# Kernel tuning notes

Measured on AMD Instinct MI355X. Metric: run time of the kernel, lower is better.

The kernel has to match this reference:

```python
import jax, jax.numpy as jnp
import numpy as np

N_NODES = 50000
N_EDGES = 600000
DIM = 128
NGC = 3
NMC = 2
B = 64
M_PER = 100
M_TOT = B * M_PER
EM = 50000
DICT = 201  # motif_dict_size + 1


def setup_inputs() -> dict:
    key = jax.random.key(0)
    ks = jax.random.split(key, 20)
    w = lambda k, s: jax.random.normal(k, s, jnp.float32) * 0.05
    x = jax.random.normal(ks[0], (N_NODES, DIM), jnp.float32)
    edge_attr = jax.random.normal(ks[1], (N_EDGES, DIM), jnp.float32)
    edge_index = jax.random.randint(ks[2], (2, N_EDGES), 0, N_NODES)
    batch = jnp.sort(jax.random.randint(ks[3], (N_NODES,), 0, B))
    node2motif = jax.random.randint(ks[4], (N_NODES,), 0, M_PER)
    num_motifs = jnp.full((B,), M_PER, dtype=jnp.int32)  # fill 'ones' * 100
    # ring over all motifs guarantees unique(motif_edge_index) == 0..M_TOT-1,
    # so the original node_idx relabel is the identity map
    ring = jnp.stack([jnp.arange(M_TOT), (jnp.arange(M_TOT) + 1) % M_TOT])
    rnd = jax.random.randint(ks[5], (2, EM - M_TOT), 0, M_TOT)
    motif_edge_index = jnp.concatenate([ring, rnd], axis=1).astype(jnp.int32)
    motifid = jax.random.randint(ks[6], (M_TOT,), 0, DICT)
    emb = w(ks[7], (DICT, DIM)).at[0].set(0.0)  # padding_idx=0 row zeroed
    return dict(
        x=x, edge_attr=edge_attr, edge_index=edge_index, batch=batch,
        node2motif=node2motif, num_motifs=num_motifs,
        motif_edge_index=motif_edge_index, motifid=motifid,
        gc_W1=w(ks[8], (NGC, DIM, DIM)), gc_b1=jnp.zeros((NGC, DIM)),
        gc_W2=w(ks[9], (NGC, DIM, DIM)), gc_b2=jnp.zeros((NGC, DIM)),
        mc_W1=w(ks[10], (NMC, DIM, DIM)), mc_b1=jnp.zeros((NMC, DIM)),
        mc_W2=w(ks[11], (NMC, DIM, DIM)), mc_b2=jnp.zeros((NMC, DIM)),
        lin_W=w(ks[12], (DIM * NGC, DIM)), lin_b=jnp.zeros((DIM,)),
        emb=emb,
    )


def reference(x, edge_attr, edge_index, batch, node2motif, num_motifs,
              motif_edge_index, motifid,
              gc_W1, gc_b1, gc_W2, gc_b2,
              mc_W1, mc_b1, mc_W2, mc_b2,
              lin_W, lin_b, emb):
    N = x.shape[0]
    src, dst = edge_index[0], edge_index[1]
    # --- GINE conv stack (eps=0, no norm, dropout=0) ---
    xg_list = []
    for i in range(NGC):
        msg = jax.nn.relu(x[src] + edge_attr)                 # [E, dim]
        agg = jax.ops.segment_sum(msg, dst, num_segments=N)   # [N, dim]
        h = x + agg
        h = jax.nn.relu(h @ gc_W1[i] + gc_b1[i]) @ gc_W2[i] + gc_b2[i]
        x = jax.nn.relu(h)
        xg_list.append(x)
    xcat = jnp.concatenate(xg_list, axis=1)                   # [N, dim*NGC]
    xg = jax.ops.segment_sum(xcat, batch, num_segments=B)     # [B, dim*NGC]
    # --- motif grouping ---
    partial = jnp.concatenate([jnp.zeros((1,), num_motifs.dtype),
                               jnp.cumsum(num_motifs)[:-1]])
    n2m = node2motif + partial[batch]                         # [N] -> motif ids
    # injective=False: motif_lin first, then pool
    xm_nodes = jax.nn.relu(xcat @ lin_W + lin_b)              # [N, dim]
    xm_h = jax.ops.segment_sum(xm_nodes, n2m, num_segments=M_TOT)
    motif_batch = jnp.repeat(jnp.arange(B), num_motifs, total_repeat_length=M_TOT)
    # motif_edge_index covers exactly 0..M_TOT-1, so relabel is identity
    msrc, mdst = motif_edge_index[0], motif_edge_index[1]
    xm_h = xm_h + emb[motifid]
    # --- GIN conv stack on motif graph ---
    xm_list = []
    h = xm_h
    for i in range(NMC):
        agg = jax.ops.segment_sum(h[msrc], mdst, num_segments=M_TOT)
        t = h + agg
        t = jax.nn.relu(t @ mc_W1[i] + mc_b1[i]) @ mc_W2[i] + mc_b2[i]
        h = jax.nn.relu(t)
        xm_list.append(h)
    xm = jnp.concatenate(xm_list, axis=1)                     # [M_TOT, dim*NMC]
    xm = jax.ops.segment_sum(xm, motif_batch, num_segments=B) # [B, dim*NMC]
    return xm, xg
```

## Files before the change

### kernel.cpp

```cpp
#include <hip/hip_runtime.h>

typedef __attribute__((ext_vector_type(8))) short bf16x8;
typedef __attribute__((ext_vector_type(4))) float f32x4;

__device__ __forceinline__ unsigned f2bf_rne(float f) {
  unsigned u = __float_as_uint(f);
  return (u + 0x7FFFu + ((u >> 16) & 1u)) >> 16;
}
__device__ __forceinline__ float bf2f(unsigned h) { return __uint_as_float(h << 16); }
__device__ __forceinline__ void split_bf(float x, unsigned& hi, unsigned& lo) {
  hi = f2bf_rne(x);
  lo = f2bf_rne(x - bf2f(hi));
}

__global__ void prep_kernel(const int* __restrict__ num_motifs,
                            const int* __restrict__ batch,
                            int N, int B,
                            int* __restrict__ partial,
                            int* __restrict__ bnd) {
  int t = threadIdx.x;
  if (t == 0) {
    int s = 0;
    for (int b = 0; b < B; ++b) { partial[b] = s; s += num_motifs[b]; }
  }
  if (t <= B) {
    int lo = 0, hi = N;
    while (lo < hi) { int mid = (lo + hi) >> 1; if (batch[mid] < t) lo = mid + 1; else hi = mid; }
    bnd[t] = lo;
  }
}

__global__ __launch_bounds__(256) void hist_kernel(const int* __restrict__ dst, int E,
                                                   int* __restrict__ counts) {
  int e = blockIdx.x * 256 + threadIdx.x;
  if (e < E) atomicAdd(&counts[dst[e]], 1);
}

__global__ __launch_bounds__(1024) void scan_kernel(const int* __restrict__ counts, int n,
                                                    int* __restrict__ base,
                                                    int* __restrict__ cursor) {
  __shared__ int part[1024];
  const int tid = threadIdx.x;
  const int chunk = (n + 1023) / 1024;
  const int lo = tid * chunk;
  const int hi = min(lo + chunk, n);
  int s = 0;
  for (int i = lo; i < hi; ++i) s += counts[i];
  part[tid] = s;
  __syncthreads();
  for (int off = 1; off < 1024; off <<= 1) {
    int v = (tid >= off) ? part[tid - off] : 0;
    __syncthreads();
    part[tid] += v;
    __syncthreads();
  }
  int run = (tid > 0) ? part[tid - 1] : 0;
  for (int i = lo; i < hi; ++i) {
    base[i] = run; cursor[i] = run;
    run += counts[i];
  }
  if (tid == 1023) base[n] = part[1023];
}

__global__ __launch_bounds__(256) void scatter_kernel(const int* __restrict__ src,
                                                      const int* __restrict__ dst, int E,
                                                      int* __restrict__ cursor,
                                                      int* __restrict__ eid_s,
                                                      int* __restrict__ src_s) {
  int e = blockIdx.x * 256 + threadIdx.x;
  if (e >= E) return;
  int d = dst[e];
  int pos = atomicAdd(&cursor[d], 1);
  eid_s[pos] = e;
  src_s[pos] = src[e];
}

__global__ __launch_bounds__(256) void nm_hist_kernel(const int* __restrict__ n2m,
                                                      const int* __restrict__ batch,
                                                      const int* __restrict__ partial, int N,
                                                      int* __restrict__ counts) {
  int n = blockIdx.x * 256 + threadIdx.x;
  if (n < N) atomicAdd(&counts[n2m[n] + partial[batch[n]]], 1);
}

__global__ __launch_bounds__(256) void nm_scatter_kernel(const int* __restrict__ n2m,
                                                         const int* __restrict__ batch,
                                                         const int* __restrict__ partial, int N,
                                                         int* __restrict__ cursor,
                                                         int* __restrict__ node_s) {
  int n = blockIdx.x * 256 + threadIdx.x;
  if (n >= N) return;
  int m = n2m[n] + partial[batch[n]];
  node_s[atomicAdd(&cursor[m], 1)] = n;
}

__global__ __launch_bounds__(128) void gine_agg_kernel(
    const float* __restrict__ x, const float* __restrict__ ea,
    const int* __restrict__ base, const int* __restrict__ eid_s,
    const int* __restrict__ src_s, float* __restrict__ h, int N) {
  const int n = blockIdx.x * 2 + (threadIdx.x >> 6);
  if (n >= N) return;
  const int d2 = (threadIdx.x & 63) * 2;
  const int e0 = base[n], e1 = base[n + 1];
  float sx = 0.f, sy = 0.f;
  int j = e0;
  for (; j + 1 < e1; j += 2) {
    int eA = eid_s[j],     sA = src_s[j];
    int eB = eid_s[j + 1], sB = src_s[j + 1];
    float2 xa = *(const float2*)&x[sA * 128 + d2];
    float2 ja = *(const float2*)&ea[(long long)eA * 128 + d2];
    float2 xb = *(const float2*)&x[sB * 128 + d2];
    float2 jb = *(const float2*)&ea[(long long)eB * 128 + d2];
    sx += fmaxf(xa.x + ja.x, 0.f) + fmaxf(xb.x + jb.x, 0.f);
    sy += fmaxf(xa.y + ja.y, 0.f) + fmaxf(xb.y + jb.y, 0.f);
  }
  if (j < e1) {
    float2 xa = *(const float2*)&x[src_s[j] * 128 + d2];
    float2 ja = *(const float2*)&ea[(long long)eid_s[j] * 128 + d2];
    sx += fmaxf(xa.x + ja.x, 0.f);
    sy += fmaxf(xa.y + ja.y, 0.f);
  }
  float2 xv = *(const float2*)&x[n * 128 + d2];
  *(float2*)&h[n * 128 + d2] = make_float2(xv.x + sx, xv.y + sy);
}

__global__ __launch_bounds__(128) void gin_agg_kernel(
    const float* __restrict__ hi, const int* __restrict__ base,
    const int* __restrict__ src_s, float* __restrict__ ho, int M) {
  const int m = blockIdx.x * 2 + (threadIdx.x >> 6);
  if (m >= M) return;
  const int d2 = (threadIdx.x & 63) * 2;
  const int e0 = base[m], e1 = base[m + 1];
  float sx = 0.f, sy = 0.f;
  int j = e0;
  for (; j + 1 < e1; j += 2) {
    float2 a = *(const float2*)&hi[src_s[j] * 128 + d2];
    float2 b = *(const float2*)&hi[src_s[j + 1] * 128 + d2];
    sx += a.x + b.x; sy += a.y + b.y;
  }
  if (j < e1) {
    float2 a = *(const float2*)&hi[src_s[j] * 128 + d2];
    sx += a.x; sy += a.y;
  }
  float2 hv = *(const float2*)&hi[m * 128 + d2];
  *(float2*)&ho[m * 128 + d2] = make_float2(hv.x + sx, hv.y + sy);
}

__global__ __launch_bounds__(128) void motif_gather_kernel(
    const float* __restrict__ xm_nodes, const int* __restrict__ mb,
    const int* __restrict__ node_s, const int* __restrict__ motifid,
    const float* __restrict__ emb, float* __restrict__ xm_h, int M) {
  const int m = blockIdx.x * 2 + (threadIdx.x >> 6);
  if (m >= M) return;
  const int d2 = (threadIdx.x & 63) * 2;
  float2 e = *(const float2*)&emb[motifid[m] * 128 + d2];
  float sx = e.x, sy = e.y;
  const int j0 = mb[m], j1 = mb[m + 1];
  int j = j0;
  for (; j + 1 < j1; j += 2) {
    float2 a = *(const float2*)&xm_nodes[(long long)node_s[j] * 128 + d2];
    float2 b = *(const float2*)&xm_nodes[(long long)node_s[j + 1] * 128 + d2];
    sx += a.x + b.x; sy += a.y + b.y;
  }
  if (j < j1) {
    float2 a = *(const float2*)&xm_nodes[(long long)node_s[j] * 128 + d2];
    sx += a.x; sy += a.y;
  }
  *(float2*)&xm_h[m * 128 + d2] = make_float2(sx, sy);
}

struct WSrc { const float* p[13]; };

__global__ __launch_bounds__(256) void convw_kernel(WSrc wsrc, ushort* __restrict__ Wf) {
  const int mat = blockIdx.x >> 2;
  const int kc  = blockIdx.x & 3;
  const float* W = wsrc.p[mat];
  const int t = threadIdx.x;
  #pragma unroll
  for (int i = 0; i < 16; ++i) {
    int o = t * 16 + i;
    int nt = o >> 9, lane = (o >> 3) & 63, j = o & 7;
    int k = kc * 32 + (lane >> 4) * 8 + j;
    int n = nt * 16 + (lane & 15);
    unsigned hi, lo;
    split_bf(W[k * 128 + n], hi, lo);
    Wf[mat * 32768 + kc * 4096 + o]         = (ushort)hi;
    Wf[mat * 32768 + 16384 + kc * 4096 + o] = (ushort)lo;
  }
}

__device__ __forceinline__ void stage_a_bf(ushort* AsH, ushort* AsL,
                                           const float* __restrict__ src,
                                           int row0, int nrows, int tid) {
  #pragma unroll
  for (int it = 0; it < 16; ++it) {
    int idx = (it * 256 + tid) * 4;
    int r = idx >> 7, k = idx & 127;
    float4 v = make_float4(0.f, 0.f, 0.f, 0.f);
    if (row0 + r < nrows) v = *(const float4*)&src[(long long)(row0 + r) * 128 + k];
    unsigned h0, l0, h1, l1, h2, l2, h3, l3;
    split_bf(v.x, h0, l0); split_bf(v.y, h1, l1);
    split_bf(v.z, h2, l2); split_bf(v.w, h3, l3);
    uint2 ph = make_uint2(h0 | (h1 << 16), h2 | (h3 << 16));
    uint2 pl = make_uint2(l0 | (l1 << 16), l2 | (l3 << 16));
    int boff = r * 256 + ((k * 2) ^ ((r & 7) << 4));
    *(uint2*)((char*)AsH + boff) = ph;
    *(uint2*)((char*)AsL + boff) = pl;
  }
}

__device__ __forceinline__ bf16x8 ld_afrag(const ushort* As, int row, int k0) {
  int boff = row * 256 + ((k0 * 2) ^ ((row & 7) << 4));
  return *(const bf16x8*)((const char*)As + boff);
}

__device__ __forceinline__ bf16x8 ld_wfrag(const ushort* Wf, int kc, int nt, int lane) {
  return ((const bf16x8*)Wf)[(kc * 8 + nt) * 64 + lane];
}

__device__ __forceinline__ void mfma_gemm(const ushort* AsH, const ushort* AsL,
                                          const ushort* WfH, const ushort* WfL,
                                          int wr, int wc, int lane, f32x4 (&acc)[4][4]) {
  #pragma unroll
  for (int kc = 0; kc < 4; ++kc) {
    const int k0 = kc * 32 + (lane >> 4) * 8;
    bf16x8 ah[4], al[4], wh[4], wl[4];
    #pragma unroll
    for (int rt = 0; rt < 4; ++rt) {
      int row = wr * 64 + rt * 16 + (lane & 15);
      ah[rt] = ld_afrag(AsH, row, k0);
      al[rt] = ld_afrag(AsL, row, k0);
    }
    #pragma unroll
    for (int ct = 0; ct < 4; ++ct) {
      int nt = wc * 4 + ct;
      wh[ct] = ld_wfrag(WfH, kc, nt, lane);
      wl[ct] = ld_wfrag(WfL, kc, nt, lane);
    }
    #pragma unroll
    for (int rt = 0; rt < 4; ++rt)
      #pragma unroll
      for (int ct = 0; ct < 4; ++ct) {
        acc[rt][ct] = __builtin_amdgcn_mfma_f32_16x16x32_bf16(ah[rt], wh[ct], acc[rt][ct], 0, 0, 0);
        acc[rt][ct] = __builtin_amdgcn_mfma_f32_16x16x32_bf16(ah[rt], wl[ct], acc[rt][ct], 0, 0, 0);
        acc[rt][ct] = __builtin_amdgcn_mfma_f32_16x16x32_bf16(al[rt], wh[ct], acc[rt][ct], 0, 0, 0);
      }
  }
}

__device__ __forceinline__ void bias_acc(f32x4 (&acc)[4][4], const float* __restrict__ b,
                                         int wc, int lane) {
  #pragma unroll
  for (int ct = 0; ct < 4; ++ct) {
    float bv = b[wc * 64 + ct * 16 + (lane & 15)];
    #pragma unroll
    for (int rt = 0; rt < 4; ++rt) acc[rt][ct] = (f32x4){bv, bv, bv, bv};
  }
}

__global__ __launch_bounds__(256, 2) void mlp_mfma_kernel(
    const float* __restrict__ h,
    const ushort* __restrict__ W1f, const float* __restrict__ b1,
    const ushort* __restrict__ W2f, const float* __restrict__ b2,
    float* __restrict__ out, int nrows) {
  __shared__ ushort AsH[128 * 128];
  __shared__ ushort AsL[128 * 128];
  const int tid = threadIdx.x;
  const int lane = tid & 63;
  const int w = tid >> 6;
  const int wr = w >> 1, wc = w & 1;
  const int row0 = blockIdx.x * 128;

  stage_a_bf(AsH, AsL, h, row0, nrows, tid);
  __syncthreads();

  f32x4 acc[4][4];
  bias_acc(acc, b1, wc, lane);
  mfma_gemm(AsH, AsL, W1f, W1f + 16384, wr, wc, lane, acc);
  __syncthreads();

  #pragma unroll
  for (int rt = 0; rt < 4; ++rt)
    #pragma unroll
    for (int ct = 0; ct < 4; ++ct) {
      int col = wc * 64 + ct * 16 + (lane & 15);
      #pragma unroll
      for (int r = 0; r < 4; ++r) {
        int row = wr * 64 + rt * 16 + (lane >> 4) * 4 + r;
        unsigned hi, lo;
        split_bf(fmaxf(acc[rt][ct][r], 0.f), hi, lo);
        int boff = row * 256 + ((col * 2) ^ ((row & 7) << 4));
        *(ushort*)((char*)AsH + boff) = (ushort)hi;
        *(ushort*)((char*)AsL + boff) = (ushort)lo;
      }
    }
  __syncthreads();

  f32x4 acc2[4][4];
  bias_acc(acc2, b2, wc, lane);
  mfma_gemm(AsH, AsL, W2f, W2f + 16384, wr, wc, lane, acc2);

  #pragma unroll
  for (int rt = 0; rt < 4; ++rt)
    #pragma unroll
    for (int ct = 0; ct < 4; ++ct) {
      int col = wc * 64 + ct * 16 + (lane & 15);
      #pragma unroll
      for (int r = 0; r < 4; ++r) {
        int row = row0 + wr * 64 + rt * 16 + (lane >> 4) * 4 + r;
        if (row < nrows) out[(long long)row * 128 + col] = fmaxf(acc2[rt][ct][r], 0.f);
      }
    }
}

__global__ __launch_bounds__(256, 2) void lin_mfma_kernel(
    const float* __restrict__ x1, const float* __restrict__ x2, const float* __restrict__ x3,
    const ushort* __restrict__ Wlf, const float* __restrict__ lb,
    float* __restrict__ xm_nodes, int nrows) {
  __shared__ ushort AsH[128 * 128];
  __shared__ ushort AsL[128 * 128];
  const int tid = threadIdx.x;
  const int lane = tid & 63;
  const int w = tid >> 6;
  const int wr = w >> 1, wc = w & 1;
  const int row0 = blockIdx.x * 128;

  f32x4 acc[4][4];
  bias_acc(acc, lb, wc, lane);

  for (int c3 = 0; c3 < 3; ++c3) {
    const float* xs = (c3 == 0) ? x1 : (c3 == 1 ? x2 : x3);
    if (c3) __syncthreads();
    stage_a_bf(AsH, AsL, xs, row0, nrows, tid);
    __syncthreads();
    const ushort* Wc = Wlf + c3 * 32768;
    mfma_gemm(AsH, AsL, Wc, Wc + 16384, wr, wc, lane, acc);
  }

  #pragma unroll
  for (int rt = 0; rt < 4; ++rt)
    #pragma unroll
    for (int ct = 0; ct < 4; ++ct) {
      int col = wc * 64 + ct * 16 + (lane & 15);
      #pragma unroll
      for (int r = 0; r < 4; ++r) {
        int row = row0 + wr * 64 + rt * 16 + (lane >> 4) * 4 + r;
        if (row < nrows) xm_nodes[(long long)row * 128 + col] = fmaxf(acc[rt][ct][r], 0.f);
      }
    }
}

__global__ __launch_bounds__(192) void xg_pool_kernel(
    const float* __restrict__ x1, const float* __restrict__ x2, const float* __restrict__ x3,
    const int* __restrict__ batch, int N, int chunk, float* __restrict__ outg) {
  const int c0 = blockIdx.x * chunk;
  if (c0 >= N) return;
  const int c1 = min(c0 + chunk, N);
  const int l = threadIdx.x >> 6;
  const int d2 = (threadIdx.x & 63) * 2;
  const float* xs = (l == 0) ? x1 : (l == 1 ? x2 : x3);
  int b = batch[c0];
  float sx = 0.f, sy = 0.f;
  for (int n = c0; n < c1; ++n) {
    int bn = batch[n];
    if (bn != b) {
      if (sx != 0.f) atomicAdd(&outg[b * 384 + l * 128 + d2], sx);
      if (sy != 0.f) atomicAdd(&outg[b * 384 + l * 128 + d2 + 1], sy);
      sx = 0.f; sy = 0.f; b = bn;
    }
    float2 v = *(const float2*)&xs[n * 128 + d2];
    sx += v.x; sy += v.y;
  }
  atomicAdd(&outg[b * 384 + l * 128 + d2], sx);
  atomicAdd(&outg[b * 384 + l * 128 + d2 + 1], sy);
}

__global__ __launch_bounds__(128) void xm_pool_kernel(
    const float* __restrict__ m1, const float* __restrict__ m2,
    const int* __restrict__ partial, int B, int M, int chunk,
    float* __restrict__ outm) {
  const int c0 = blockIdx.x * chunk;
  if (c0 >= M) return;
  const int c1 = min(c0 + chunk, M);
  const int l = threadIdx.x >> 6;
  const int d2 = (threadIdx.x & 63) * 2;
  const float* ms = (l == 0) ? m1 : m2;
  int b = 0;
  while (b + 1 < B && partial[b + 1] <= c0) ++b;
  int bend = (b + 1 < B) ? partial[b + 1] : M;
  float sx = 0.f, sy = 0.f;
  for (int m = c0; m < c1; ++m) {
    if (m >= bend) {
      if (sx != 0.f) atomicAdd(&outm[b * 256 + l * 128 + d2], sx);
      if (sy != 0.f) atomicAdd(&outm[b * 256 + l * 128 + d2 + 1], sy);
      sx = 0.f; sy = 0.f;
      do { ++b; } while (b + 1 < B && partial[b + 1] <= m);
      bend = (b + 1 < B) ? partial[b + 1] : M;
    }
    float2 v = *(const float2*)&ms[m * 128 + d2];
    sx += v.x; sy += v.y;
  }
  atomicAdd(&outm[b * 256 + l * 128 + d2], sx);
  atomicAdd(&outm[b * 256 + l * 128 + d2 + 1], sy);
}

extern "C" void kernel_launch(void* const* d_in, const int* in_sizes, int n_in,
                              void* d_out, int out_size, void* d_ws, size_t ws_size,
                              hipStream_t stream) {
  const float* x       = (const float*)d_in[0];
  const float* ea      = (const float*)d_in[1];
  const int*   eidx    = (const int*)d_in[2];
  const int*   batch   = (const int*)d_in[3];
  const int*   n2m     = (const int*)d_in[4];
  const int*   nmot    = (const int*)d_in[5];
  const int*   meidx   = (const int*)d_in[6];
  const int*   motifid = (const int*)d_in[7];
  const float* gcW1 = (const float*)d_in[8];
  const float* gcb1 = (const float*)d_in[9];
  const float* gcW2 = (const float*)d_in[10];
  const float* gcb2 = (const float*)d_in[11];
  const float* mcW1 = (const float*)d_in[12];
  const float* mcb1 = (const float*)d_in[13];
  const float* mcW2 = (const float*)d_in[14];
  const float* mcb2 = (const float*)d_in[15];
  const float* linW = (const float*)d_in[16];
  const float* linb = (const float*)d_in[17];
  const float* emb  = (const float*)d_in[18];
  float* outp = (float*)d_out;

  const int N  = in_sizes[0] / 128;
  const int E  = in_sizes[1] / 128;
  const int B  = in_sizes[5];
  const int ME = in_sizes[6] / 2;
  const int M  = in_sizes[7];

  const size_t nodeBytes = (size_t)N * 128 * 4;
  const size_t motBytes  = (size_t)M * 128 * 4;
  char* ws = (char*)d_ws;
  float* xl0 = (float*)ws;                 ws += nodeBytes;
  float* xl1 = (float*)ws;                 ws += nodeBytes;
  float* xl2 = (float*)ws;                 ws += nodeBytes;
  char*  R   = ws;                         ws += nodeBytes;
  ushort* Wf = (ushort*)ws;                ws += (size_t)13 * 32768 * 2;
  int* counts  = (int*)ws;                 ws += (size_t)N * 4;
  int* base    = (int*)ws;                 ws += (size_t)(N + 1) * 4;
  int* cursor  = (int*)ws;                 ws += (size_t)N * 4;
  int* eid_s   = (int*)ws;                 ws += (size_t)E * 4;
  int* src_s   = (int*)ws;                 ws += (size_t)E * 4;
  int* mcounts = (int*)ws;                 ws += (size_t)M * 4;
  int* mbase   = (int*)ws;                 ws += (size_t)(M + 1) * 4;
  int* mcursor = (int*)ws;                 ws += (size_t)M * 4;
  int* meid_s  = (int*)ws;                 ws += (size_t)ME * 4;
  int* msrc_s  = (int*)ws;                 ws += (size_t)ME * 4;
  int* nmcnt   = (int*)ws;                 ws += (size_t)M * 4;
  int* nmbase  = (int*)ws;                 ws += (size_t)(M + 1) * 4;
  int* nmcur   = (int*)ws;                 ws += (size_t)M * 4;
  int* node_s  = (int*)ws;                 ws += (size_t)N * 4;
  int* partial = (int*)ws;                 ws += 256;
  int* bnd     = (int*)ws;                 ws += 512;
  if ((size_t)(ws - (char*)d_ws) > ws_size) return;

  float* hbuf     = (float*)R;
  float* xm_nodes = (float*)R;
  float* xmh = (float*)((char*)xl0);
  float* hm  = (float*)((char*)xl0 + motBytes);
  float* ml0 = (float*)((char*)xl0 + 2 * motBytes);
  float* ml1 = (float*)((char*)xl0 + 3 * motBytes);

  hipMemsetAsync(outp, 0, (size_t)out_size * 4, stream);

  prep_kernel<<<1, 128, 0, stream>>>(nmot, batch, N, B, partial, bnd);

  WSrc wsrc;
  wsrc.p[0] = gcW1;            wsrc.p[1] = gcW1 + 16384;  wsrc.p[2] = gcW1 + 32768;
  wsrc.p[3] = gcW2;            wsrc.p[4] = gcW2 + 16384;  wsrc.p[5] = gcW2 + 32768;
  wsrc.p[6] = mcW1;            wsrc.p[7] = mcW1 + 16384;
  wsrc.p[8] = mcW2;            wsrc.p[9] = mcW2 + 16384;
  wsrc.p[10] = linW;           wsrc.p[11] = linW + 16384; wsrc.p[12] = linW + 32768;
  convw_kernel<<<52, 256, 0, stream>>>(wsrc, Wf);

  const int* src = eidx;
  const int* dst = eidx + E;
  hipMemsetAsync(counts, 0, (size_t)N * 4, stream);
  hist_kernel<<<(E + 255) / 256, 256, 0, stream>>>(dst, E, counts);
  scan_kernel<<<1, 1024, 0, stream>>>(counts, N, base, cursor);
  scatter_kernel<<<(E + 255) / 256, 256, 0, stream>>>(src, dst, E, cursor, eid_s, src_s);

  const int* msrc = meidx;
  const int* mdst = meidx + ME;
  hipMemsetAsync(mcounts, 0, (size_t)M * 4, stream);
  hist_kernel<<<(ME + 255) / 256, 256, 0, stream>>>(mdst, ME, mcounts);
  scan_kernel<<<1, 1024, 0, stream>>>(mcounts, M, mbase, mcursor);
  scatter_kernel<<<(ME + 255) / 256, 256, 0, stream>>>(msrc, mdst, ME, mcursor, meid_s, msrc_s);

  hipMemsetAsync(nmcnt, 0, (size_t)M * 4, stream);
  nm_hist_kernel<<<(N + 255) / 256, 256, 0, stream>>>(n2m, batch, partial, N, nmcnt);
  scan_kernel<<<1, 1024, 0, stream>>>(nmcnt, M, nmbase, nmcur);
  nm_scatter_kernel<<<(N + 255) / 256, 256, 0, stream>>>(n2m, batch, partial, N, nmcur, node_s);

  const float* xs[3] = {x, xl0, xl1};
  float* xo[3] = {xl0, xl1, xl2};
  const int ngrid = (N + 127) / 128;
  for (int i = 0; i < 3; ++i) {
    gine_agg_kernel<<<(N + 1) / 2, 128, 0, stream>>>(xs[i], ea, base, eid_s, src_s, hbuf, N);
    mlp_mfma_kernel<<<ngrid, 256, 0, stream>>>(hbuf,
        Wf + (size_t)(0 + i) * 32768, gcb1 + i * 128,
        Wf + (size_t)(3 + i) * 32768, gcb2 + i * 128, xo[i], N);
  }
  {
    const int nb = 512;
    const int chunk = (N + nb - 1) / nb;
    xg_pool_kernel<<<nb, 192, 0, stream>>>(xl0, xl1, xl2, batch, N, chunk, outp + B * 256);
  }

  lin_mfma_kernel<<<ngrid, 256, 0, stream>>>(xl0, xl1, xl2, Wf + (size_t)10 * 32768, linb,
                                             xm_nodes, N);
  motif_gather_kernel<<<(M + 1) / 2, 128, 0, stream>>>(xm_nodes, nmbase, node_s,
                                                       motifid, emb, xmh, M);

  const float* hs[2] = {xmh, ml0};
  float* mo[2] = {ml0, ml1};
  const int mgrid = (M + 127) / 128;
  for (int i = 0; i < 2; ++i) {
    gin_agg_kernel<<<(M + 1) / 2, 128, 0, stream>>>(hs[i], mbase, msrc_s, hm, M);
    mlp_mfma_kernel<<<mgrid, 256, 0, stream>>>(hm,
        Wf + (size_t)(6 + i) * 32768, mcb1 + i * 128,
        Wf + (size_t)(8 + i) * 32768, mcb2 + i * 128, mo[i], M);
  }
  {
    const int nb = 256;
    const int chunk = (M + nb - 1) / nb;
    xm_pool_kernel<<<nb, 128, 0, stream>>>(ml0, ml1, partial, B, M, chunk, outp);
  }
}
```

Baseline: 1.125 ms.

## Permute edge attributes into CSR order once and reuse across GINE layers

On the first GINE layer, the aggregation kernel writes each gathered edge_attr row into a dst-sorted buffer. Layers two and three then read that buffer sequentially instead of gathering rows by edge id, and unroll the loop by four. Edge id and source index are packed into one int2 array. This turns two random 307MB-scale gathers into streaming reads, at the cost of an extra 307MB write and workspace in the first layer.

```diff
diff --git a/kernel.cpp b/kernel.cpp
--- a/kernel.cpp
+++ b/kernel.cpp
@@ -65,14 +65,12 @@
 __global__ __launch_bounds__(256) void scatter_kernel(const int* __restrict__ src,
                                                       const int* __restrict__ dst, int E,
                                                       int* __restrict__ cursor,
-                                                      int* __restrict__ eid_s,
-                                                      int* __restrict__ src_s) {
+                                                      int2* __restrict__ ed_s) {
   int e = blockIdx.x * 256 + threadIdx.x;
   if (e >= E) return;
   int d = dst[e];
   int pos = atomicAdd(&cursor[d], 1);
-  eid_s[pos] = e;
-  src_s[pos] = src[e];
+  ed_s[pos] = make_int2(e, src[e]);
 }
 
 __global__ __launch_bounds__(256) void nm_hist_kernel(const int* __restrict__ n2m,
@@ -94,10 +92,10 @@
   node_s[atomicAdd(&cursor[m], 1)] = n;
 }
 
-__global__ __launch_bounds__(128) void gine_agg_kernel(
+__global__ __launch_bounds__(128) void gine_first_kernel(
     const float* __restrict__ x, const float* __restrict__ ea,
-    const int* __restrict__ base, const int* __restrict__ eid_s,
-    const int* __restrict__ src_s, float* __restrict__ h, int N) {
+    const int* __restrict__ base, const int2* __restrict__ ed_s,
+    float* __restrict__ ea_s, float* __restrict__ h, int N) {
   const int n = blockIdx.x * 2 + (threadIdx.x >> 6);
   if (n >= N) return;
   const int d2 = (threadIdx.x & 63) * 2;
@@ -105,18 +103,21 @@
   float sx = 0.f, sy = 0.f;
   int j = e0;
   for (; j + 1 < e1; j += 2) {
-    int eA = eid_s[j],     sA = src_s[j];
-    int eB = eid_s[j + 1], sB = src_s[j + 1];
-    float2 xa = *(const float2*)&x[sA * 128 + d2];
-    float2 ja = *(const float2*)&ea[(long long)eA * 128 + d2];
-    float2 xb = *(const float2*)&x[sB * 128 + d2];
-    float2 jb = *(const float2*)&ea[(long long)eB * 128 + d2];
+    int2 eA = ed_s[j], eB = ed_s[j + 1];
+    float2 ja = *(const float2*)&ea[(long long)eA.x * 128 + d2];
+    float2 jb = *(const float2*)&ea[(long long)eB.x * 128 + d2];
+    float2 xa = *(const float2*)&x[eA.y * 128 + d2];
+    float2 xb = *(const float2*)&x[eB.y * 128 + d2];
+    *(float2*)&ea_s[(long long)j * 128 + d2] = ja;
+    *(float2*)&ea_s[(long long)(j + 1) * 128 + d2] = jb;
     sx += fmaxf(xa.x + ja.x, 0.f) + fmaxf(xb.x + jb.x, 0.f);
     sy += fmaxf(xa.y + ja.y, 0.f) + fmaxf(xb.y + jb.y, 0.f);
   }
   if (j < e1) {
-    float2 xa = *(const float2*)&x[src_s[j] * 128 + d2];
-    float2 ja = *(const float2*)&ea[(long long)eid_s[j] * 128 + d2];
+    int2 eA = ed_s[j];
+    float2 ja = *(const float2*)&ea[(long long)eA.x * 128 + d2];
+    float2 xa = *(const float2*)&x[eA.y * 128 + d2];
+    *(float2*)&ea_s[(long long)j * 128 + d2] = ja;
     sx += fmaxf(xa.x + ja.x, 0.f);
     sy += fmaxf(xa.y + ja.y, 0.f);
   }
@@ -124,9 +125,45 @@
   *(float2*)&h[n * 128 + d2] = make_float2(xv.x + sx, xv.y + sy);
 }
 
+__global__ __launch_bounds__(128) void gine_rest_kernel(
+    const float* __restrict__ x, const float* __restrict__ ea_s,
+    const int* __restrict__ base, const int2* __restrict__ ed_s,
+    float* __restrict__ h, int N) {
+  const int n = blockIdx.x * 2 + (threadIdx.x >> 6);
+  if (n >= N) return;
+  const int d2 = (threadIdx.x & 63) * 2;
+  const int e0 = base[n], e1 = base[n + 1];
+  float sx = 0.f, sy = 0.f;
+  int j = e0;
+  for (; j + 3 < e1; j += 4) {
+    int s0 = ed_s[j].y, s1 = ed_s[j + 1].y, s2 = ed_s[j + 2].y, s3 = ed_s[j + 3].y;
+    float2 j0 = *(const float2*)&ea_s[(long long)j * 128 + d2];
+    float2 j1 = *(const float2*)&ea_s[(long long)(j + 1) * 128 + d2];
+    float2 j2 = *(const float2*)&ea_s[(long long)(j + 2) * 128 + d2];
+    float2 j3 = *(const float2*)&ea_s[(long long)(j + 3) * 128 + d2];
+    float2 x0 = *(const float2*)&x[s0 * 128 + d2];
+    float2 x1 = *(const float2*)&x[s1 * 128 + d2];
+    float2 x2 = *(const float2*)&x[s2 * 128 + d2];
+    float2 x3 = *(const float2*)&x[s3 * 128 + d2];
+    sx += fmaxf(x0.x + j0.x, 0.f) + fmaxf(x1.x + j1.x, 0.f)
+        + fmaxf(x2.x + j2.x, 0.f) + fmaxf(x3.x + j3.x, 0.f);
+    sy += fmaxf(x0.y + j0.y, 0.f) + fmaxf(x1.y + j1.y, 0.f)
+        + fmaxf(x2.y + j2.y, 0.f) + fmaxf(x3.y + j3.y, 0.f);
+  }
+  for (; j < e1; ++j) {
+    int s0 = ed_s[j].y;
+    float2 j0 = *(const float2*)&ea_s[(long long)j * 128 + d2];
+    float2 x0 = *(const float2*)&x[s0 * 128 + d2];
+    sx += fmaxf(x0.x + j0.x, 0.f);
+    sy += fmaxf(x0.y + j0.y, 0.f);
+  }
+  float2 xv = *(const float2*)&x[n * 128 + d2];
+  *(float2*)&h[n * 128 + d2] = make_float2(xv.x + sx, xv.y + sy);
+}
+
 __global__ __launch_bounds__(128) void gin_agg_kernel(
     const float* __restrict__ hi, const int* __restrict__ base,
-    const int* __restrict__ src_s, float* __restrict__ ho, int M) {
+    const int2* __restrict__ ed_s, float* __restrict__ ho, int M) {
   const int m = blockIdx.x * 2 + (threadIdx.x >> 6);
   if (m >= M) return;
   const int d2 = (threadIdx.x & 63) * 2;
@@ -134,12 +171,12 @@
   float sx = 0.f, sy = 0.f;
   int j = e0;
   for (; j + 1 < e1; j += 2) {
-    float2 a = *(const float2*)&hi[src_s[j] * 128 + d2];
-    float2 b = *(const float2*)&hi[src_s[j + 1] * 128 + d2];
+    float2 a = *(const float2*)&hi[ed_s[j].y * 128 + d2];
+    float2 b = *(const float2*)&hi[ed_s[j + 1].y * 128 + d2];
     sx += a.x + b.x; sy += a.y + b.y;
   }
   if (j < e1) {
-    float2 a = *(const float2*)&hi[src_s[j] * 128 + d2];
+    float2 a = *(const float2*)&hi[ed_s[j].y * 128 + d2];
     sx += a.x; sy += a.y;
   }
   float2 hv = *(const float2*)&hi[m * 128 + d2];
@@ -441,17 +478,16 @@
   float* xl1 = (float*)ws;                 ws += nodeBytes;
   float* xl2 = (float*)ws;                 ws += nodeBytes;
   char*  R   = ws;                         ws += nodeBytes;
+  float* ea_s = (float*)ws;                ws += (size_t)E * 128 * 4;
   ushort* Wf = (ushort*)ws;                ws += (size_t)13 * 32768 * 2;
   int* counts  = (int*)ws;                 ws += (size_t)N * 4;
   int* base    = (int*)ws;                 ws += (size_t)(N + 1) * 4;
   int* cursor  = (int*)ws;                 ws += (size_t)N * 4;
-  int* eid_s   = (int*)ws;                 ws += (size_t)E * 4;
-  int* src_s   = (int*)ws;                 ws += (size_t)E * 4;
+  int2* ed_s   = (int2*)ws;                ws += (size_t)E * 8;
   int* mcounts = (int*)ws;                 ws += (size_t)M * 4;
   int* mbase   = (int*)ws;                 ws += (size_t)(M + 1) * 4;
   int* mcursor = (int*)ws;                 ws += (size_t)M * 4;
-  int* meid_s  = (int*)ws;                 ws += (size_t)ME * 4;
-  int* msrc_s  = (int*)ws;                 ws += (size_t)ME * 4;
+  int2* med_s  = (int2*)ws;                ws += (size_t)ME * 8;
   int* nmcnt   = (int*)ws;                 ws += (size_t)M * 4;
   int* nmbase  = (int*)ws;                 ws += (size_t)(M + 1) * 4;
   int* nmcur   = (int*)ws;                 ws += (size_t)M * 4;
@@ -484,25 +520,27 @@
   hipMemsetAsync(counts, 0, (size_t)N * 4, stream);
   hist_kernel<<<(E + 255) / 256, 256, 0, stream>>>(dst, E, counts);
   scan_kernel<<<1, 1024, 0, stream>>>(counts, N, base, cursor);
-  scatter_kernel<<<(E + 255) / 256, 256, 0, stream>>>(src, dst, E, cursor, eid_s, src_s);
+  scatter_kernel<<<(E + 255) / 256, 256, 0, stream>>>(src, dst, E, cursor, ed_s);
 
   const int* msrc = meidx;
   const int* mdst = meidx + ME;
   hipMemsetAsync(mcounts, 0, (size_t)M * 4, stream);
   hist_kernel<<<(ME + 255) / 256, 256, 0, stream>>>(mdst, ME, mcounts);
   scan_kernel<<<1, 1024, 0, stream>>>(mcounts, M, mbase, mcursor);
-  scatter_kernel<<<(ME + 255) / 256, 256, 0, stream>>>(msrc, mdst, ME, mcursor, meid_s, msrc_s);
+  scatter_kernel<<<(ME + 255) / 256, 256, 0, stream>>>(msrc, mdst, ME, mcursor, med_s);
 
   hipMemsetAsync(nmcnt, 0, (size_t)M * 4, stream);
   nm_hist_kernel<<<(N + 255) / 256, 256, 0, stream>>>(n2m, batch, partial, N, nmcnt);
   scan_kernel<<<1, 1024, 0, stream>>>(nmcnt, M, nmbase, nmcur);
   nm_scatter_kernel<<<(N + 255) / 256, 256, 0, stream>>>(n2m, batch, partial, N, nmcur, node_s);
 
-  const float* xs[3] = {x, xl0, xl1};
   float* xo[3] = {xl0, xl1, xl2};
   const int ngrid = (N + 127) / 128;
-  for (int i = 0; i < 3; ++i) {
-    gine_agg_kernel<<<(N + 1) / 2, 128, 0, stream>>>(xs[i], ea, base, eid_s, src_s, hbuf, N);
+  gine_first_kernel<<<(N + 1) / 2, 128, 0, stream>>>(x, ea, base, ed_s, ea_s, hbuf, N);
+  mlp_mfma_kernel<<<ngrid, 256, 0, stream>>>(hbuf,
+      Wf + (size_t)0 * 32768, gcb1, Wf + (size_t)3 * 32768, gcb2, xl0, N);
+  for (int i = 1; i < 3; ++i) {
+    gine_rest_kernel<<<(N + 1) / 2, 128, 0, stream>>>(xo[i - 1], ea_s, base, ed_s, hbuf, N);
     mlp_mfma_kernel<<<ngrid, 256, 0, stream>>>(hbuf,
         Wf + (size_t)(0 + i) * 32768, gcb1 + i * 128,
         Wf + (size_t)(3 + i) * 32768, gcb2 + i * 128, xo[i], N);
@@ -522,7 +560,7 @@
   float* mo[2] = {ml0, ml1};
   const int mgrid = (M + 127) / 128;
   for (int i = 0; i < 2; ++i) {
-    gin_agg_kernel<<<(M + 1) / 2, 128, 0, stream>>>(hs[i], mbase, msrc_s, hm, M);
+    gin_agg_kernel<<<(M + 1) / 2, 128, 0, stream>>>(hs[i], mbase, med_s, hm, M);
     mlp_mfma_kernel<<<mgrid, 256, 0, stream>>>(hm,
         Wf + (size_t)(6 + i) * 32768, mcb1 + i * 128,
         Wf + (size_t)(8 + i) * 32768, mcb2 + i * 128, mo[i], M);
```

New measurement: 1.162 ms. +3.2%, slower.
